# Performance work log

Measured on AMD Instinct MI355X. Metric: run time of the kernel, lower is better.

## Reference

```python
import jax, jax.numpy as jnp
from jax import lax
import numpy as np

STRIDE = 1
PADDING = 1
THRESHOLD = 0.25
DECAY = 0.9


def setup_inputs() -> dict:
    key = jax.random.key(0)
    k1, k2 = jax.random.split(key)
    B, Cin, L, T = 16, 32, 1024, 64
    Cout, K = 64, 3
    x = jax.random.uniform(k1, (B, Cin, L, T), dtype=jnp.float32)
    weight = jax.random.normal(k2, (Cout, Cin, K), dtype=jnp.float32) * 0.1
    return {"x": x, "weight": weight}


def reference(x, weight):
    # x: (B, Cin, L, T); weight: (Cout, Cin, K)
    B, Cin, L, T = x.shape
    Cout, _, K = weight.shape
    # Conv1d applied to every timestep at once: fold T into the batch dim.
    xt = jnp.transpose(x, (0, 3, 1, 2)).reshape(B * T, Cin, L)  # (B*T, Cin, L)
    act = lax.conv_general_dilated(
        xt, weight,
        window_strides=(STRIDE,),
        padding=[(PADDING, PADDING)],
        dimension_numbers=("NCH", "OIH", "NCH"),
    )  # (B*T, Cout, OL)
    OL = act.shape[-1]
    act = act.reshape(B, T, Cout, OL).transpose(1, 0, 2, 3)  # (T, B, Cout, OL)

    def step(pot, a):
        # LIF update: integrate, decay, threshold, reset (matches original order).
        pot = (pot + a) * DECAY
        spk = (pot >= THRESHOLD).astype(pot.dtype)
        pot = jnp.where(spk > 0, jnp.zeros_like(pot), pot)
        return pot, spk

    pot0 = jnp.zeros((B, Cout, OL), dtype=x.dtype)
    _, spikes = lax.scan(step, pot0, act)  # spikes: (T, B, Cout, OL)
    return jnp.transpose(spikes, (1, 2, 3, 0))  # (B, Cout, OL, T)
```

## Files before the change

kernel.cpp:

```cpp
#include <hip/hip_runtime.h>

#define BB    16
#define CIN   32
#define LEN   1024
#define TT    64
#define COUT  64
#define KK    3

#define TL       16
#define HALO     (TL + 2)
#define NTHREADS 512
#define NGRAN    (CIN * HALO * 4)
#define NROUND   (NGRAN / 64)


__device__ float wpk2[COUT * CIN * KK];
__device__ float zeros_g[64];

__global__ void repack_w(const float* __restrict__ w) {
    const int i = blockIdx.x * 256 + threadIdx.x;
    if (i < COUT * CIN * KK) {
        const int j  = i & 7;
        const int ci = (i >> 3) & 31;
        const int gk = i >> 8;
        const int k  = gk % 3;
        const int g2 = gk / 3;
        wpk2[i] = w[((g2 * 8 + j) * CIN + ci) * KK + k];
    }
}

#define GLD16(GP, LP) __builtin_amdgcn_global_load_lds(                      \
    (const __attribute__((address_space(1))) void*)(GP),                     \
    (__attribute__((address_space(3))) void*)(LP), 16, 0, 0)

__global__ __launch_bounds__(NTHREADS, 4)
void snn_v6(const float* __restrict__ x, float* __restrict__ out) {
    __shared__ float4 xsg[2][NGRAN];

    const int tid  = threadIdx.x;
    const int l    = tid & 15;
    const int tsub = (tid >> 4) & 3;
    const int lane = tid & 63;
    const int wv   = __builtin_amdgcn_readfirstlane(tid >> 6);
    const int l0   = blockIdx.x * TL;
    const int b    = blockIdx.y;
    const int lo   = l0 + l;

    const float* xb   = x + (size_t)b * CIN * LEN * TT;
    float*       outb = out + (size_t)b * COUT * LEN * TT;
    const float* wgb  = wpk2 + wv * (KK * CIN * 8);

    const float* src[5];
    #pragma unroll
    for (int m = 0; m < 5; ++m) {
        const float* p = zeros_g;
        const int r = wv + 8 * m;
        if (r < NROUND) {
            const int G   = r * 64 + lane;
            const int ci  = G / (HALO * 4);
            const int rem = G - ci * (HALO * 4);
            const int row = rem >> 2;
            const int h   = rem & 3;
            const int lg  = l0 - 1 + row;
            if (lg >= 0 && lg < LEN)
                p = xb + ((size_t)ci * LEN + lg) * TT + h * 4;
        }
        src[m] = p;
    }

    auto issue = [&](int tc, int buf) {
        char* lb = (char*)&xsg[buf][0];
        #pragma unroll
        for (int m = 0; m < 4; ++m)
            GLD16(src[m] + tc * 16, lb + (wv + 8 * m) * 1024);
        if (wv < 4)
            GLD16(src[4] + tc * 16, lb + (wv + 32) * 1024);
    };

    float pot[8];
    #pragma unroll
    for (int j = 0; j < 8; ++j) pot[j] = 0.f;
    unsigned nibp = 0;

    issue(0, 0);

    #pragma unroll 2
    for (int tc = 0; tc < 4; ++tc) {
        const int cur = tc & 1;
        __syncthreads();
        if (tc + 1 < 4) issue(tc + 1, cur ^ 1);

        const char* xsv = (const char*)&xsg[cur][0] + tsub * 16;

        float acc[8][4];
        #pragma unroll
        for (int j = 0; j < 8; ++j)
            #pragma unroll
            for (int i = 0; i < 4; ++i) acc[j][i] = 0.f;

        #pragma unroll
        for (int k = 0; k < KK; ++k) {
            const char*  bk = xsv + (l + k) * 64;
            const float* wk = wgb + k * (CIN * 8);
            #pragma unroll 1
            for (int cic = 0; cic < 4; ++cic) {
                #pragma unroll
                for (int c8 = 0; c8 < 8; ++c8) {
                    const int ci = cic * 8 + c8;
                    const float4 xr = *(const float4*)(bk + ci * 1152);
                    const float* wp = wk + ci * 8;
                    #pragma unroll
                    for (int j = 0; j < 8; ++j) {
                        const float wj = wp[j];
                        acc[j][0] = fmaf(xr.x, wj, acc[j][0]);
                        acc[j][1] = fmaf(xr.y, wj, acc[j][1]);
                        acc[j][2] = fmaf(xr.z, wj, acc[j][2]);
                        acc[j][3] = fmaf(xr.w, wj, acc[j][3]);
                    }
                }
            }
        }

        unsigned nibc = 0;
        #pragma unroll
        for (int ph = 0; ph < 4; ++ph) {
            const int srcl = (((ph + 3) & 3) << 4) | l;
            #pragma unroll
            for (int j = 0; j < 8; ++j) {
                const float pin = __shfl(pot[j], srcl, 64);
                if (tsub == ph) {
                    float pp = pin;
                    unsigned sb = 0;
                    #pragma unroll
                    for (int i = 0; i < 4; ++i) {
                        const float s  = pp + acc[j][i];
                        const float p  = s * 0.9f;
                        const bool  sp = (p >= 0.25f);
                        sb |= sp ? (1u << i) : 0u;
                        pp = sp ? 0.f : p;
                    }
                    pot[j] = pp;
                    nibc |= sb << (j * 4);
                }
            }
        }

        if (cur) {
            #pragma unroll
            for (int j = 0; j < 8; ++j) {
                float* dst = outb + ((size_t)(wv * 8 + j) * LEN + lo) * TT
                           + (tc - 1) * 16 + tsub * 4;
                const unsigned n0 = (nibp >> (j * 4)) & 0xFu;
                const unsigned n1 = (nibc >> (j * 4)) & 0xFu;
                *(float4*)dst = make_float4(n0 & 1u ? 1.f : 0.f,
                                            n0 & 2u ? 1.f : 0.f,
                                            n0 & 4u ? 1.f : 0.f,
                                            n0 & 8u ? 1.f : 0.f);
                *(float4*)(dst + 16) = make_float4(n1 & 1u ? 1.f : 0.f,
                                                   n1 & 2u ? 1.f : 0.f,
                                                   n1 & 4u ? 1.f : 0.f,
                                                   n1 & 8u ? 1.f : 0.f);
            }
        } else {
            nibp = nibc;
        }
    }
}

extern "C" void kernel_launch(void* const* d_in, const int* in_sizes, int n_in,
                              void* d_out, int out_size, void* d_ws, size_t ws_size,
                              hipStream_t stream) {
    const float* x = (const float*)d_in[0];
    const float* w = (const float*)d_in[1];
    float* out = (float*)d_out;
    (void)d_ws; (void)ws_size; (void)in_sizes; (void)n_in; (void)out_size;

    hipLaunchKernelGGL(repack_w, dim3(24), dim3(256), 0, stream, w);
    hipLaunchKernelGGL(snn_v6, dim3(LEN / TL, BB), dim3(NTHREADS),
                       0, stream, x, out);
}
```

Baseline: 721.2 us.

## Restructure SNN kernel: 128-thread blocks, serial time chunks, swizzled LDS, deferred stores

```diff
diff --git a/kernel.cpp b/kernel.cpp
--- a/kernel.cpp
+++ b/kernel.cpp
@@ -8,13 +8,13 @@
 #define KK    3
 
 #define TL       16
-#define HALO     (TL + 2)
-#define NTHREADS 512
+#define HALO     18
+#define NTHREADS 128
 #define NGRAN    (CIN * HALO * 4)
-#define NROUND   (NGRAN / 64)
+#define RPT      18
 
 
-__device__ float wpk2[COUT * CIN * KK];
+__device__ float wpk8[COUT * CIN * KK];
 __device__ float zeros_g[64];
 
 __global__ void repack_w(const float* __restrict__ w) {
@@ -24,8 +24,8 @@
         const int ci = (i >> 3) & 31;
         const int gk = i >> 8;
         const int k  = gk % 3;
-        const int g2 = gk / 3;
-        wpk2[i] = w[((g2 * 8 + j) * CIN + ci) * KK + k];
+        const int g  = gk / 3;
+        wpk8[i] = w[((g * 8 + j) * CIN + ci) * KK + k];
     }
 }
 
@@ -33,136 +33,151 @@
     (const __attribute__((address_space(1))) void*)(GP),                     \
     (__attribute__((address_space(3))) void*)(LP), 16, 0, 0)
 
-__global__ __launch_bounds__(NTHREADS, 4)
-void snn_v6(const float* __restrict__ x, float* __restrict__ out) {
-    __shared__ float4 xsg[2][NGRAN];
+__global__ __launch_bounds__(NTHREADS, 2)
+void snn_v8(const float* __restrict__ x, float* __restrict__ out) {
+    __shared__ float4 xs[NGRAN];
 
     const int tid  = threadIdx.x;
-    const int l    = tid & 15;
-    const int tsub = (tid >> 4) & 3;
+    const int g    = (tid >> 3) & 7;
+    const int l    = (tid & 7) | ((tid >> 6) << 3);
     const int lane = tid & 63;
     const int wv   = __builtin_amdgcn_readfirstlane(tid >> 6);
-    const int l0   = blockIdx.x * TL;
-    const int b    = blockIdx.y;
-    const int lo   = l0 + l;
 
-    const float* xb   = x + (size_t)b * CIN * LEN * TT;
+    const int lin = blockIdx.x;
+    const int wid = (lin & 7) * 128 + (lin >> 3);
+    const int b   = wid >> 6;
+    const int lx  = wid & 63;
+    const int l0  = lx * TL;
+    const int lo  = l0 + l;
+
+    const float* xb   = x   + (size_t)b * CIN * LEN * TT;
     float*       outb = out + (size_t)b * COUT * LEN * TT;
-    const float* wgb  = wpk2 + wv * (KK * CIN * 8);
 
-    const float* src[5];
+    int goff[RPT];
+    unsigned okm = 0u;
     #pragma unroll
-    for (int m = 0; m < 5; ++m) {
-        const float* p = zeros_g;
-        const int r = wv + 8 * m;
-        if (r < NROUND) {
-            const int G   = r * 64 + lane;
-            const int ci  = G / (HALO * 4);
-            const int rem = G - ci * (HALO * 4);
-            const int row = rem >> 2;
-            const int h   = rem & 3;
-            const int lg  = l0 - 1 + row;
-            if (lg >= 0 && lg < LEN)
-                p = xb + ((size_t)ci * LEN + lg) * TT + h * 4;
-        }
-        src[m] = p;
+    for (int m = 0; m < RPT; ++m) {
+        const int G   = (wv * RPT + m) * 64 + lane;
+        const int ci  = G / (HALO * 4);
+        const int rem = G - ci * (HALO * 4);
+        const int row = rem >> 2;
+        const int gp  = rem & 3;
+        const int ts  = gp ^ (row & 3);
+        const int lg  = l0 - 1 + row;
+        const bool ok = (lg >= 0) && (lg < LEN);
+        okm |= ok ? (1u << m) : 0u;
+        goff[m] = (ci * LEN + (ok ? lg : 0)) * TT + ts * 4;
     }
 
-    auto issue = [&](int tc, int buf) {
-        char* lb = (char*)&xsg[buf][0];
+    float    pot[8];
+    unsigned blo[8], bhi[8];
+    #pragma unroll
+    for (int j = 0; j < 8; ++j) { pot[j] = 0.f; blo[j] = 0u; bhi[j] = 0u; }
+
+    const float* wg  = wpk8 + g * (KK * CIN * 8);
+    const char*  xsb = (const char*)xs;
+
+    #pragma unroll 1
+    for (int sc = 0; sc < 4; ++sc) {
+        if (sc) __syncthreads();
+        {
+            char* lb = (char*)xs + (wv * RPT) * 1024;
+            #pragma unroll
+            for (int m = 0; m < RPT; ++m) {
+                const float* sp = (okm & (1u << m)) ? (xb + goff[m] + sc * 16)
+                                                    : zeros_g;
+                GLD16(sp, lb + m * 1024);
+            }
+        }
+        __syncthreads();
+
+        unsigned stb[8];
         #pragma unroll
-        for (int m = 0; m < 4; ++m)
-            GLD16(src[m] + tc * 16, lb + (wv + 8 * m) * 1024);
-        if (wv < 4)
-            GLD16(src[4] + tc * 16, lb + (wv + 32) * 1024);
-    };
+        for (int j = 0; j < 8; ++j) stb[j] = 0u;
 
-    float pot[8];
-    #pragma unroll
-    for (int j = 0; j < 8; ++j) pot[j] = 0.f;
-    unsigned nibp = 0;
+        auto subpass = [&](int s2) {
+            float acc[8][8];
+            #pragma unroll
+            for (int j = 0; j < 8; ++j)
+                #pragma unroll
+                for (int i = 0; i < 8; ++i) acc[j][i] = 0.f;
 
-    issue(0, 0);
-
-    #pragma unroll 2
-    for (int tc = 0; tc < 4; ++tc) {
-        const int cur = tc & 1;
-        __syncthreads();
-        if (tc + 1 < 4) issue(tc + 1, cur ^ 1);
-
-        const char* xsv = (const char*)&xsg[cur][0] + tsub * 16;
-
-        float acc[8][4];
-        #pragma unroll
-        for (int j = 0; j < 8; ++j)
-            #pragma unroll
-            for (int i = 0; i < 4; ++i) acc[j][i] = 0.f;
-
-        #pragma unroll
-        for (int k = 0; k < KK; ++k) {
-            const char*  bk = xsv + (l + k) * 64;
-            const float* wk = wgb + k * (CIN * 8);
             #pragma unroll 1
-            for (int cic = 0; cic < 4; ++cic) {
-                #pragma unroll
-                for (int c8 = 0; c8 < 8; ++c8) {
-                    const int ci = cic * 8 + c8;
-                    const float4 xr = *(const float4*)(bk + ci * 1152);
-                    const float* wp = wk + ci * 8;
+            for (int k = 0; k < KK; ++k) {
+                const int rowk = l + k;
+                const int sw   = rowk & 3;
+                const char* a0 = xsb + rowk * 64 + (((s2 * 2 + 0) ^ sw) << 4);
+                const char* a1 = xsb + rowk * 64 + (((s2 * 2 + 1) ^ sw) << 4);
+                const float* wk = wg + k * (CIN * 8);
+                #pragma unroll 1
+                for (int cic = 0; cic < 4; ++cic) {
                     #pragma unroll
-                    for (int j = 0; j < 8; ++j) {
-                        const float wj = wp[j];
-                        acc[j][0] = fmaf(xr.x, wj, acc[j][0]);
-                        acc[j][1] = fmaf(xr.y, wj, acc[j][1]);
-                        acc[j][2] = fmaf(xr.z, wj, acc[j][2]);
-                        acc[j][3] = fmaf(xr.w, wj, acc[j][3]);
+                    for (int c8 = 0; c8 < 8; ++c8) {
+                        const int ci = cic * 8 + c8;
+                        const float4 x0 = *(const float4*)(a0 + ci * 1152);
+                        const float4 x1 = *(const float4*)(a1 + ci * 1152);
+                        const float4 wa = *(const float4*)(wk + ci * 8);
+                        const float4 wb = *(const float4*)(wk + ci * 8 + 4);
+                        #pragma unroll
+                        for (int j = 0; j < 8; ++j) {
+                            const float w = (j == 0) ? wa.x : (j == 1) ? wa.y
+                                          : (j == 2) ? wa.z : (j == 3) ? wa.w
+                                          : (j == 4) ? wb.x : (j == 5) ? wb.y
+                                          : (j == 6) ? wb.z : wb.w;
+                            acc[j][0] = fmaf(x0.x, w, acc[j][0]);
+                            acc[j][1] = fmaf(x0.y, w, acc[j][1]);
+                            acc[j][2] = fmaf(x0.z, w, acc[j][2]);
+                            acc[j][3] = fmaf(x0.w, w, acc[j][3]);
+                            acc[j][4] = fmaf(x1.x, w, acc[j][4]);
+                            acc[j][5] = fmaf(x1.y, w, acc[j][5]);
+                            acc[j][6] = fmaf(x1.z, w, acc[j][6]);
+                            acc[j][7] = fmaf(x1.w, w, acc[j][7]);
+                        }
                     }
                 }
             }
-        }
 
-        unsigned nibc = 0;
-        #pragma unroll
-        for (int ph = 0; ph < 4; ++ph) {
-            const int srcl = (((ph + 3) & 3) << 4) | l;
             #pragma unroll
             for (int j = 0; j < 8; ++j) {
-                const float pin = __shfl(pot[j], srcl, 64);
-                if (tsub == ph) {
-                    float pp = pin;
-                    unsigned sb = 0;
-                    #pragma unroll
-                    for (int i = 0; i < 4; ++i) {
-                        const float s  = pp + acc[j][i];
-                        const float p  = s * 0.9f;
-                        const bool  sp = (p >= 0.25f);
-                        sb |= sp ? (1u << i) : 0u;
-                        pp = sp ? 0.f : p;
-                    }
-                    pot[j] = pp;
-                    nibc |= sb << (j * 4);
+                float p = pot[j];
+                unsigned sb = 0u;
+                #pragma unroll
+                for (int i = 0; i < 8; ++i) {
+                    const float s  = p + acc[j][i];
+                    const float q  = s * 0.9f;
+                    const bool  sp = (q >= 0.25f);
+                    sb |= sp ? (1u << (s2 * 8 + i)) : 0u;
+                    p = sp ? 0.f : q;
                 }
+                pot[j] = p;
+                stb[j] |= sb;
             }
+        };
+        subpass(0);
+        subpass(1);
+
+        const unsigned sh = (unsigned)((sc & 1) * 16);
+        if (sc < 2) {
+            #pragma unroll
+            for (int j = 0; j < 8; ++j) blo[j] |= stb[j] << sh;
+        } else {
+            #pragma unroll
+            for (int j = 0; j < 8; ++j) bhi[j] |= stb[j] << sh;
         }
+    }
 
-        if (cur) {
-            #pragma unroll
-            for (int j = 0; j < 8; ++j) {
-                float* dst = outb + ((size_t)(wv * 8 + j) * LEN + lo) * TT
-                           + (tc - 1) * 16 + tsub * 4;
-                const unsigned n0 = (nibp >> (j * 4)) & 0xFu;
-                const unsigned n1 = (nibc >> (j * 4)) & 0xFu;
-                *(float4*)dst = make_float4(n0 & 1u ? 1.f : 0.f,
-                                            n0 & 2u ? 1.f : 0.f,
-                                            n0 & 4u ? 1.f : 0.f,
-                                            n0 & 8u ? 1.f : 0.f);
-                *(float4*)(dst + 16) = make_float4(n1 & 1u ? 1.f : 0.f,
-                                                   n1 & 2u ? 1.f : 0.f,
-                                                   n1 & 4u ? 1.f : 0.f,
-                                                   n1 & 8u ? 1.f : 0.f);
-            }
-        } else {
-            nibp = nibc;
+    #pragma unroll
+    for (int j = 0; j < 8; ++j) {
+        float* dst = outb + ((size_t)(g * 8 + j) * LEN + lo) * TT;
+        const unsigned wlo = blo[j], whi = bhi[j];
+        #pragma unroll
+        for (int q = 0; q < 16; ++q) {
+            const unsigned word = (q < 8) ? wlo : whi;
+            const unsigned nib  = word >> ((q & 7) * 4);
+            *(float4*)(dst + q * 4) = make_float4(nib & 1u ? 1.f : 0.f,
+                                                  nib & 2u ? 1.f : 0.f,
+                                                  nib & 4u ? 1.f : 0.f,
+                                                  nib & 8u ? 1.f : 0.f);
         }
     }
 }
@@ -176,6 +191,6 @@
     (void)d_ws; (void)ws_size; (void)in_sizes; (void)n_in; (void)out_size;
 
     hipLaunchKernelGGL(repack_w, dim3(24), dim3(256), 0, stream, w);
-    hipLaunchKernelGGL(snn_v6, dim3(LEN / TL, BB), dim3(NTHREADS),
+    hipLaunchKernelGGL(snn_v8, dim3((LEN / TL) * BB), dim3(NTHREADS),
                        0, stream, x, out);
 }
```

Measured after the change: 713.3 us. About the same (-1.1%).
